# Optimization experiments

Hardware: AMD Instinct MI355X
Metric: run time of the kernel (lower is better)

## Reference

```python
import jax, jax.numpy as jnp
import numpy as np

B, N, H, D, L = 4, 1024, 8, 256, 4
SVD, NSP = 16, 512
DK = D // H
EPS = 1e-6


def setup_inputs() -> dict:
    key = jax.random.key(0)
    ks = jax.random.split(key, 40)
    p = {}
    p["x"] = jax.random.normal(ks[0], (B, N, D), jnp.float32)
    p["in_degrees"] = jax.random.randint(ks[1], (N,), 0, N)
    p["out_degrees"] = jax.random.randint(ks[2], (N,), 0, N)
    p["spatial_pos"] = jax.random.randint(ks[3], (N, N), 0, NSP)
    p["svd_emb"] = jax.random.normal(ks[4], (N, 2 * SVD), jnp.float32)
    # embedding tables (padding_idx=0 -> zero row)
    p["in_deg_emb"] = (0.02 * jax.random.normal(ks[5], (N, D), jnp.float32)).at[0].set(0.0)
    p["out_deg_emb"] = (0.02 * jax.random.normal(ks[6], (N, D), jnp.float32)).at[0].set(0.0)
    p["spatial_emb"] = (0.02 * jax.random.normal(ks[7], (NSP, H), jnp.float32)).at[0].set(0.0)
    # SVD linear (stored [in, out]; y = x @ W + b)
    p["W_svd"] = 0.02 * jax.random.normal(ks[8], (2 * SVD, D), jnp.float32)
    p["b_svd"] = jnp.zeros((D,), jnp.float32)
    # per-layer stacked transformer params
    names = ["Wq", "Wk", "Wv", "Wa", "W1", "W2"]
    for i, nm in enumerate(names):
        p[nm] = 0.05 * jax.random.normal(ks[9 + i], (L, D, D), jnp.float32)
    for nm in ["bq", "bk", "bv", "ba", "b1", "b2", "ln1_b", "ln2_b"]:
        p[nm] = jnp.zeros((L, D), jnp.float32)
    p["ln1_g"] = jnp.ones((L, D), jnp.float32)
    p["ln2_g"] = jnp.ones((L, D), jnp.float32)
    return p


def _ln(x, g, b):
    mu = jnp.mean(x, axis=-1, keepdims=True)
    var = jnp.mean(jnp.square(x - mu), axis=-1, keepdims=True)
    return (x - mu) * jax.lax.rsqrt(var + EPS) * g + b


def _forward(x, svd_emb, W_svd, b_svd, in_deg_emb, out_deg_emb, spatial_emb,
             Wq, bq, Wk, bk, Wv, bv, Wa, ba, ln1_g, ln1_b,
             W1, b1, W2, b2, ln2_g, ln2_b,
             in_degrees, out_degrees, spatial_pos):
    # node-level: degree embeddings ([N,D] broadcasts over batch)
    x = x + in_deg_emb[in_degrees] + out_deg_emb[out_degrees]
    # node-level: SVD embedding (deterministic sign = +1 -> concat(u, -v))
    pos = jnp.concatenate([svd_emb[:, :SVD], -svd_emb[:, SVD:]], axis=-1)
    x = x + pos @ W_svd + b_svd
    # attention-level spatial bias: [N,N,H] -> [H,N,N], broadcast over batch
    attn_bias = jnp.transpose(spatial_emb[spatial_pos], (2, 0, 1))
    scale = 1.0 / jnp.sqrt(jnp.asarray(DK, x.dtype))

    def body(h, params):
        wq, bq_, wk, bk_, wv, bv_, wa, ba_, g1, b1_, w1, bb1, w2, bb2, g2, b2_ = params
        q = (h @ wq + bq_).reshape(B, N, H, DK)
        k = (h @ wk + bk_).reshape(B, N, H, DK)
        v = (h @ wv + bv_).reshape(B, N, H, DK)
        # scores [B,H,N,N] + spatial bias [H,N,N]
        scores = jnp.einsum('bqhd,bkhd->bhqk', q, k) * scale + attn_bias
        attn = jax.nn.softmax(scores, axis=-1)
        o = jnp.einsum('bhqk,bkhd->bqhd', attn, v).reshape(B, N, D)
        h = _ln(h + o @ wa + ba_, g1, b1_)
        f = jnp.maximum(h @ w1 + bb1, 0.0) @ w2 + bb2
        h = _ln(h + f, g2, b2_)
        return h, None

    x, _ = jax.lax.scan(body, x, (Wq, bq, Wk, bk, Wv, bv, Wa, ba, ln1_g, ln1_b,
                                  W1, b1, W2, b2, ln2_g, ln2_b))
    return x


def reference(x, svd_emb, W_svd, b_svd, in_deg_emb, out_deg_emb, spatial_emb,
              Wq, bq, Wk, bk, Wv, bv, Wa, ba, ln1_g, ln1_b,
              W1, b1, W2, b2, ln2_g, ln2_b,
              in_degrees, out_degrees, spatial_pos):
    return _forward(x, svd_emb, W_svd, b_svd, in_deg_emb, out_deg_emb, spatial_emb,
                    Wq, bq, Wk, bk, Wv, bv, Wa, ba, ln1_g, ln1_b,
                    W1, b1, W2, b2, ln2_g, ln2_b,
                    in_degrees, out_degrees, spatial_pos)
```

## Files before the change

kernel.cpp:

```cpp
#include <hip/hip_runtime.h>
#include <hip/hip_bf16.h>
#include <math.h>

#define NN 1024
#define BB 4
#define HH 8
#define DD 256
#define LL 4
#define DKK 32
#define MM 4096
#define EPSF 1e-6f
#define LOG2EF 1.4426950408889634f
#define SCLOG2E 0.2550348625f

typedef __attribute__((ext_vector_type(8))) short short8;
typedef __attribute__((ext_vector_type(4))) float f32x4;
typedef unsigned int u32;

__device__ __forceinline__ unsigned short f2bf(float f) {
    __hip_bfloat16 h = __float2bfloat16(f);
    return *(unsigned short*)&h;
}
__device__ __forceinline__ float bf2f(unsigned short u) {
    unsigned v = ((unsigned)u) << 16;
    return __builtin_bit_cast(float, v);
}

__global__ __launch_bounds__(256) void init_kernel(
    const float* __restrict__ x, const int* __restrict__ deg_in,
    const int* __restrict__ deg_out, const float* __restrict__ svd,
    const float* __restrict__ in_emb, const float* __restrict__ out_emb,
    const float* __restrict__ Wsvd, const float* __restrict__ bsvd,
    const float* __restrict__ Wq, const float* __restrict__ Wk,
    const float* __restrict__ Wv, const float* __restrict__ Wa,
    const float* __restrict__ W1, const float* __restrict__ W2,
    const int* __restrict__ sp, const float* __restrict__ spemb,
    float* __restrict__ h, short* __restrict__ hb,
    short* __restrict__ Wt, short* __restrict__ bsw)
{
    int blk = blockIdx.x;
    int tid = threadIdx.x;
    {
        int n = blk & (NN - 1);
        int di = deg_in[n], dou = deg_out[n];
        float acc = x[(size_t)blk * DD + tid] + in_emb[(size_t)di * DD + tid]
                  + out_emb[(size_t)dou * DD + tid] + bsvd[tid];
        const float* sv = &svd[n * 32];
#pragma unroll
        for (int j = 0; j < 32; ++j) {
            float v = sv[j];
            v = (j < 16) ? v : -v;
            acc += v * Wsvd[j * DD + tid];
        }
        h[(size_t)blk * DD + tid] = acc;
        hb[(size_t)blk * DD + tid] = (short)f2bf(acc);
    }
    if (blk < 384) {
        __shared__ float t[64][65];
        int z = blk >> 4, tile = blk & 15;
        int name = z >> 2;
        const float* srcs[6] = {Wq, Wk, Wv, Wa, W1, W2};
        const float* W = srcs[name] + (size_t)(z & 3) * DD * DD;
        short* dst = Wt + (size_t)z * DD * DD;
        int r0 = (tile >> 2) * 64, c0 = (tile & 3) * 64;
#pragma unroll
        for (int i = 0; i < 16; ++i) {
            int idx = i * 256 + tid;
            int r = idx >> 6, cc = idx & 63;
            t[r][cc] = W[(size_t)(r0 + r) * DD + c0 + cc];
        }
        __syncthreads();
#pragma unroll
        for (int i = 0; i < 16; ++i) {
            int idx = i * 256 + tid;
            int n = idx >> 6, kk = idx & 63;
            dst[(size_t)(c0 + n) * DD + r0 + kk] = (short)f2bf(t[kk][n]);
        }
    } else if (blk < 1408) {
        int bb = blk - 384;
        int part = bb & 3;
        int tt = (bb >> 2) * 256 + tid;
        int ln = tt & 63, kt = (tt >> 6) & 15, q16 = tt >> 10;
        int qd = ln >> 4, cc = ln & 15;
        int row = q16 * 16 + cc;
        unsigned buf[8][2];
#pragma unroll
        for (int r = 0; r < 4; ++r) {
            int colj = kt * 64 + part * 16 + qd * 4 + r;
            int pp = sp[row * NN + colj];
            float4 e0 = *(const float4*)&spemb[pp * 8];
            float4 e1 = *(const float4*)&spemb[pp * 8 + 4];
            float ev[8] = {e0.x, e0.y, e0.z, e0.w, e1.x, e1.y, e1.z, e1.w};
#pragma unroll
            for (int hh = 0; hh < 8; ++hh) {
                unsigned short u = f2bf(ev[hh] * LOG2EF);
                if (r & 1) buf[hh][r >> 1] |= ((unsigned)u) << 16;
                else       buf[hh][r >> 1] = u;
            }
        }
#pragma unroll
        for (int hh = 0; hh < 8; ++hh) {
            uint2* dst = (uint2*)&bsw[(((size_t)hh * 64 + q16) * 16 + kt) * 1024
                                      + (size_t)ln * 16 + part * 4];
            *dst = make_uint2(buf[hh][0], buf[hh][1]);
        }
    }
}

__global__ __launch_bounds__(256) void gemm_qkv_kernel(
    const short* __restrict__ A,
    const short* __restrict__ Wtq, const short* __restrict__ Wtk,
    const short* __restrict__ Wtv,
    const float* __restrict__ bq, const float* __restrict__ bk,
    const float* __restrict__ bv,
    short* __restrict__ qo, short* __restrict__ ko, short* __restrict__ vo)
{
    int z = blockIdx.z;
    const short* Wt = (z == 0) ? Wtq : (z == 1) ? Wtk : Wtv;
    const float* bs = (z == 0) ? bq : (z == 1) ? bk : bv;
    int tid = threadIdx.x, wave = tid >> 6, lane = tid & 63;
    int quad = lane >> 4, c = lane & 15;
    int m0 = blockIdx.x * 16;
    int n0 = blockIdx.y * 64 + wave * 16;
    f32x4 acc = {0.f, 0.f, 0.f, 0.f};
    const short* Ap = &A[(size_t)(m0 + c) * DD];
#pragma unroll
    for (int ks = 0; ks < 8; ++ks) {
        short8 af = *(const short8*)&Ap[ks * 32 + quad * 8];
        short8 bf = *(const short8*)&Wt[(size_t)(n0 + c) * DD + ks * 32 + quad * 8];
        acc = __builtin_amdgcn_mfma_f32_16x16x32_bf16(af, bf, acc, 0, 0, 0);
    }
    int b = m0 >> 10;
    int tok0 = (m0 & (NN - 1)) + quad * 4;
    int col = n0 + c;
    int head = col >> 5, dk = col & 31;
    int bh = b * 8 + head;
    float bv2 = bs[col];
    if (z == 2) {
        ushort4 pk;
        pk.x = f2bf(acc[0] + bv2); pk.y = f2bf(acc[1] + bv2);
        pk.z = f2bf(acc[2] + bv2); pk.w = f2bf(acc[3] + bv2);
        *(ushort4*)&vo[((size_t)bh * DKK + dk) * NN + tok0] = pk;
    } else {
        short* out = (z == 0) ? qo : ko;
        float sc = (z == 0) ? SCLOG2E : 1.0f;
#pragma unroll
        for (int r = 0; r < 4; ++r)
            out[((size_t)bh * NN + tok0 + r) * DKK + dk] =
                (short)f2bf((acc[r] + bv2) * sc);
    }
}

__global__ __launch_bounds__(256) void attn_kernel(
    const short* __restrict__ q, const short* __restrict__ k,
    const short* __restrict__ vt, const short* __restrict__ bsw,
    short* __restrict__ obuf)
{
    int blk = blockIdx.x;
    int head = blk & 7;
    int b = (blk >> 3) & 3;
    int qg = blk >> 5;
    int tid = threadIdx.x, wave = tid >> 6, lane = tid & 63;
    int quad = lane >> 4, c = lane & 15;
    int bh = b * 8 + head;
    int qt = qg * 4 + wave;
    int q0 = qt * 16;
    int m0 = b * NN + q0;

    __shared__ short Ks[2][64][32];
    __shared__ short Vs[2][32][64];
    __shared__ short P[4][16][72];
    const f32x4 zero = {0.f, 0.f, 0.f, 0.f};

    auto stage = [&](int t, int buf) {
        const short* ksrc = &k[((size_t)bh * NN + t * 64 + wave * 16 + (lane >> 2)) * DKK
                               + (lane & 3) * 8];
        __builtin_amdgcn_global_load_lds(
            (const __attribute__((address_space(1))) u32*)ksrc,
            (__attribute__((address_space(3))) u32*)&Ks[buf][wave * 16][0], 16, 0, 0);
        const short* vsrc = &vt[((size_t)bh * DKK + wave * 8 + (lane >> 3)) * NN
                                + t * 64 + (lane & 7) * 8];
        __builtin_amdgcn_global_load_lds(
            (const __attribute__((address_space(1))) u32*)vsrc,
            (__attribute__((address_space(3))) u32*)&Vs[buf][wave * 8][0], 16, 0, 0);
    };

    stage(0, 0);

    short8 qf = *(const short8*)&q[((size_t)bh * NN + q0 + c) * DKK + quad * 8];
    const short* bbase = &bsw[(((size_t)head * 64 + qt) * 16) * 1024 + (size_t)lane * 16];
    short8 bc0 = *(const short8*)bbase;
    short8 bc1 = *(const short8*)(bbase + 8);

    f32x4 Oa0 = zero, Oa1 = zero;
    float lsum = 0.f;

    __syncthreads();

    for (int kti = 0; kti < 16; ++kti) {
        int cur = kti & 1;
        if (kti < 15) stage(kti + 1, cur ^ 1);
        short8 kf[4];
#pragma unroll
        for (int f = 0; f < 4; ++f)
            kf[f] = *(const short8*)&Ks[cur][f * 16 + c][quad * 8];
        short8 vf0[2], vf1[2];
#pragma unroll
        for (int kc = 0; kc < 2; ++kc) {
            vf0[kc] = *(const short8*)&Vs[cur][c][kc * 32 + quad * 8];
            vf1[kc] = *(const short8*)&Vs[cur][16 + c][kc * 32 + quad * 8];
        }
        f32x4 s[4];
#pragma unroll
        for (int f = 0; f < 4; ++f)
            s[f] = __builtin_amdgcn_mfma_f32_16x16x32_bf16(kf[f], qf, zero, 0, 0, 0);
        short8 bn0 = bc0, bn1 = bc1;
        if (kti < 15) {
            const short* bp = bbase + (size_t)(kti + 1) * 1024;
            bn0 = *(const short8*)bp;
            bn1 = *(const short8*)(bp + 8);
        }
#pragma unroll
        for (int f = 0; f < 4; ++f) {
            ushort4 pk;
#pragma unroll
            for (int r = 0; r < 4; ++r) {
                int jj = f * 4 + r;
                unsigned short uu = (unsigned short)((jj < 8) ? bc0[jj] : bc1[jj - 8]);
                float p = __builtin_amdgcn_exp2f(s[f][r] + bf2f(uu));
                lsum += p;
                unsigned short pb = f2bf(p);
                if (r == 0) pk.x = pb; else if (r == 1) pk.y = pb;
                else if (r == 2) pk.z = pb; else pk.w = pb;
            }
            *(ushort4*)&P[wave][c][f * 16 + quad * 4] = pk;
        }
        bc0 = bn0; bc1 = bn1;
#pragma unroll
        for (int kc = 0; kc < 2; ++kc) {
            short8 pf = *(const short8*)&P[wave][c][kc * 32 + quad * 8];
            Oa0 = __builtin_amdgcn_mfma_f32_16x16x32_bf16(pf, vf0[kc], Oa0, 0, 0, 0);
            Oa1 = __builtin_amdgcn_mfma_f32_16x16x32_bf16(pf, vf1[kc], Oa1, 0, 0, 0);
        }
        __syncthreads();
    }
    lsum += __shfl_xor(lsum, 16);
    lsum += __shfl_xor(lsum, 32);
#pragma unroll
    for (int r = 0; r < 4; ++r) {
        int rr = quad * 4 + r;
        float invl = 1.0f / __shfl(lsum, rr);
        obuf[(size_t)(m0 + rr) * DD + head * 32 + c]      = (short)f2bf(Oa0[r] * invl);
        obuf[(size_t)(m0 + rr) * DD + head * 32 + 16 + c] = (short)f2bf(Oa1[r] * invl);
    }
}

template <int QKV>
__global__ __launch_bounds__(512) void post_kernel(
    const short* __restrict__ obuf,
    const short* __restrict__ Wta, const short* __restrict__ Wt1,
    const short* __restrict__ Wt2,
    const float* __restrict__ ba, const float* __restrict__ b1,
    const float* __restrict__ b2,
    const float* __restrict__ g1, const float* __restrict__ lb1,
    const float* __restrict__ g2, const float* __restrict__ lb2,
    float* __restrict__ h,
    const short* __restrict__ Wtqn, const short* __restrict__ Wtkn,
    const short* __restrict__ Wtvn,
    const float* __restrict__ bqn, const float* __restrict__ bkn,
    const float* __restrict__ bvn,
    short* __restrict__ qo, short* __restrict__ ko, short* __restrict__ vo)
{
    int tid = threadIdx.x, wave = tid >> 6, lane = tid & 63;
    int quad = lane >> 4, c = lane & 15;
    int m0 = blockIdx.x * 16;
    int b = m0 >> 10;
    int q0 = m0 & (NN - 1);
    int nb = wave * 32;

    __shared__ short t_in[16][264];
    __shared__ short t1s[16][264];
    __shared__ float shs[8][16][2];
    const f32x4 zero = {0.f, 0.f, 0.f, 0.f};

    {
        int row = tid >> 5, cg = tid & 31;
        *(short8*)&t_in[row][cg * 8] = *(const short8*)&obuf[(size_t)(m0 + row) * DD + cg * 8];
    }
    __syncthreads();

    f32x4 acc[2] = {zero, zero};
#pragma unroll
    for (int ks = 0; ks < 8; ++ks) {
        short8 af = *(const short8*)&t_in[c][ks * 32 + quad * 8];
#pragma unroll
        for (int f = 0; f < 2; ++f) {
            short8 bf = *(const short8*)&Wta[(size_t)(nb + f * 16 + c) * DD + ks * 32 + quad * 8];
            acc[f] = __builtin_amdgcn_mfma_f32_16x16x32_bf16(af, bf, acc[f], 0, 0, 0);
        }
    }
    float val[2][4];
    float ps[4] = {0.f,0.f,0.f,0.f}, ps2[4] = {0.f,0.f,0.f,0.f};
#pragma unroll
    for (int f = 0; f < 2; ++f) {
        int col = nb + f * 16 + c;
        float bv = ba[col];
#pragma unroll
        for (int r = 0; r < 4; ++r) {
            float v = h[(size_t)(m0 + quad * 4 + r) * DD + col] + acc[f][r] + bv;
            val[f][r] = v;
            ps[r] += v;
            ps2[r] += v * v;
        }
    }
#pragma unroll
    for (int r = 0; r < 4; ++r)
#pragma unroll
        for (int off = 1; off < 16; off <<= 1) {
            ps[r]  += __shfl_xor(ps[r], off);
            ps2[r] += __shfl_xor(ps2[r], off);
        }
    if (c == 0)
#pragma unroll
        for (int r = 0; r < 4; ++r) {
            shs[wave][quad * 4 + r][0] = ps[r];
            shs[wave][quad * 4 + r][1] = ps2[r];
        }
    __syncthreads();
    float res[2][4];
#pragma unroll
    for (int r = 0; r < 4; ++r) {
        int rr = quad * 4 + r;
        float ts = 0.f, t2 = 0.f;
#pragma unroll
        for (int w = 0; w < 8; ++w) { ts += shs[w][rr][0]; t2 += shs[w][rr][1]; }
        float mu = ts * (1.0f / DD);
        float rv = rsqrtf(t2 * (1.0f / DD) - mu * mu + EPSF);
#pragma unroll
        for (int f = 0; f < 2; ++f) {
            int col = nb + f * 16 + c;
            float nv = (val[f][r] - mu) * rv * g1[col] + lb1[col];
            res[f][r] = nv;
            t_in[rr][col] = (short)f2bf(nv);
        }
    }
    __syncthreads();
#pragma unroll
    for (int f = 0; f < 2; ++f) {
        int n0 = nb + f * 16;
        f32x4 a1 = zero;
#pragma unroll
        for (int ks = 0; ks < 8; ++ks) {
            short8 af = *(const short8*)&t_in[c][ks * 32 + quad * 8];
            short8 bf = *(const short8*)&Wt1[(size_t)(n0 + c) * DD + ks * 32 + quad * 8];
            a1 = __builtin_amdgcn_mfma_f32_16x16x32_bf16(af, bf, a1, 0, 0, 0);
        }
        float bv = b1[n0 + c];
#pragma unroll
        for (int r = 0; r < 4; ++r)
            t1s[quad * 4 + r][n0 + c] = (short)f2bf(fmaxf(a1[r] + bv, 0.f));
    }
    __syncthreads();
    f32x4 acc2[2] = {zero, zero};
#pragma unroll
    for (int ks = 0; ks < 8; ++ks) {
        short8 af = *(const short8*)&t1s[c][ks * 32 + quad * 8];
#pragma unroll
        for (int f = 0; f < 2; ++f) {
            short8 bf = *(const short8*)&Wt2[(size_t)(nb + f * 16 + c) * DD + ks * 32 + quad * 8];
            acc2[f] = __builtin_amdgcn_mfma_f32_16x16x32_bf16(af, bf, acc2[f], 0, 0, 0);
        }
    }
    float ps_2[4] = {0.f,0.f,0.f,0.f}, ps2_2[4] = {0.f,0.f,0.f,0.f};
#pragma unroll
    for (int f = 0; f < 2; ++f) {
        int col = nb + f * 16 + c;
        float bv = b2[col];
#pragma unroll
        for (int r = 0; r < 4; ++r) {
            float v = res[f][r] + acc2[f][r] + bv;
            val[f][r] = v;
            ps_2[r] += v;
            ps2_2[r] += v * v;
        }
    }
#pragma unroll
    for (int r = 0; r < 4; ++r)
#pragma unroll
        for (int off = 1; off < 16; off <<= 1) {
            ps_2[r]  += __shfl_xor(ps_2[r], off);
            ps2_2[r] += __shfl_xor(ps2_2[r], off);
        }
    __syncthreads();
    if (c == 0)
#pragma unroll
        for (int r = 0; r < 4; ++r) {
            shs[wave][quad * 4 + r][0] = ps_2[r];
            shs[wave][quad * 4 + r][1] = ps2_2[r];
        }
    __syncthreads();
#pragma unroll
    for (int r = 0; r < 4; ++r) {
        int rr = quad * 4 + r;
        float ts = 0.f, t2 = 0.f;
#pragma unroll
        for (int w = 0; w < 8; ++w) { ts += shs[w][rr][0]; t2 += shs[w][rr][1]; }
        float mu = ts * (1.0f / DD);
        float rv = rsqrtf(t2 * (1.0f / DD) - mu * mu + EPSF);
#pragma unroll
        for (int f = 0; f < 2; ++f) {
            int col = nb + f * 16 + c;
            float nv = (val[f][r] - mu) * rv * g2[col] + lb2[col];
            h[(size_t)(m0 + rr) * DD + col] = nv;
            t_in[rr][col] = (short)f2bf(nv);
        }
    }
    if (QKV == 0) return;
    __syncthreads();
    {
        int tok0 = q0 + quad * 4;
        const short* Wz[3] = {Wtqn, Wtkn, Wtvn};
        const float* bz[3] = {bqn, bkn, bvn};
#pragma unroll
        for (int z = 0; z < 3; ++z) {
#pragma unroll
            for (int f = 0; f < 2; ++f) {
                int n0 = nb + f * 16;
                f32x4 aq = zero;
#pragma unroll
                for (int ks = 0; ks < 8; ++ks) {
                    short8 af = *(const short8*)&t_in[c][ks * 32 + quad * 8];
                    short8 bf = *(const short8*)&Wz[z][(size_t)(n0 + c) * DD + ks * 32 + quad * 8];
                    aq = __builtin_amdgcn_mfma_f32_16x16x32_bf16(af, bf, aq, 0, 0, 0);
                }
                int col = n0 + c;
                int hd = col >> 5, dk = col & 31;
                int bh2 = b * 8 + hd;
                float bv2 = bz[z][col];
                if (z == 2) {
                    ushort4 pk;
                    pk.x = f2bf(aq[0] + bv2); pk.y = f2bf(aq[1] + bv2);
                    pk.z = f2bf(aq[2] + bv2); pk.w = f2bf(aq[3] + bv2);
                    *(ushort4*)&vo[((size_t)bh2 * DKK + dk) * NN + tok0] = pk;
                } else {
                    short* out = (z == 0) ? qo : ko;
                    float sc = (z == 0) ? SCLOG2E : 1.0f;
#pragma unroll
                    for (int r = 0; r < 4; ++r)
                        out[((size_t)bh2 * NN + tok0 + r) * DKK + dk] =
                            (short)f2bf((aq[r] + bv2) * sc);
                }
            }
        }
    }
}

extern "C" void kernel_launch(void* const* d_in, const int* in_sizes, int n_in,
                              void* d_out, int out_size, void* d_ws, size_t ws_size,
                              hipStream_t stream)
{
    const float* x       = (const float*)d_in[0];
    const int*   deg_in  = (const int*)d_in[1];
    const int*   deg_out = (const int*)d_in[2];
    const int*   sp      = (const int*)d_in[3];
    const float* svd     = (const float*)d_in[4];
    const float* in_emb  = (const float*)d_in[5];
    const float* out_emb = (const float*)d_in[6];
    const float* spemb   = (const float*)d_in[7];
    const float* Wsvd    = (const float*)d_in[8];
    const float* bsvd    = (const float*)d_in[9];
    const float* Wq = (const float*)d_in[10];
    const float* Wk = (const float*)d_in[11];
    const float* Wv = (const float*)d_in[12];
    const float* Wa = (const float*)d_in[13];
    const float* W1 = (const float*)d_in[14];
    const float* W2 = (const float*)d_in[15];
    const float* bq = (const float*)d_in[16];
    const float* bk = (const float*)d_in[17];
    const float* bv = (const float*)d_in[18];
    const float* ba = (const float*)d_in[19];
    const float* b1 = (const float*)d_in[20];
    const float* b2 = (const float*)d_in[21];
    const float* ln1b = (const float*)d_in[22];
    const float* ln2b = (const float*)d_in[23];
    const float* ln1g = (const float*)d_in[24];
    const float* ln2g = (const float*)d_in[25];

    float* h = (float*)d_out;
    char*  ws = (char*)d_ws;
    short* bias = (short*)ws;
    short* qb   = (short*)(ws + ((size_t)16 << 20));
    short* kb   = (short*)(ws + ((size_t)18 << 20));
    short* vtb  = (short*)(ws + ((size_t)20 << 20));
    short* obuf = (short*)(ws + ((size_t)22 << 20));
    short* hb   = (short*)(ws + ((size_t)26 << 20));
    short* Wt   = (short*)(ws + ((size_t)28 << 20));

    init_kernel<<<MM, 256, 0, stream>>>(x, deg_in, deg_out, svd, in_emb,
        out_emb, Wsvd, bsvd, Wq, Wk, Wv, Wa, W1, W2, sp, spemb, h, hb, Wt, bias);

    const size_t WSZ = (size_t)DD * DD;
    gemm_qkv_kernel<<<dim3(MM / 16, 4, 3), 256, 0, stream>>>(
        hb, Wt + 0 * WSZ, Wt + 4 * WSZ, Wt + 8 * WSZ, bq, bk, bv, qb, kb, vtb);

    for (int l = 0; l < LL; ++l) {
        const size_t bo = (size_t)l * DD;
        const short* Wta = Wt + (3 * 4 + l) * WSZ;
        const short* Wt1 = Wt + (4 * 4 + l) * WSZ;
        const short* Wt2 = Wt + (5 * 4 + l) * WSZ;

        attn_kernel<<<512, 256, 0, stream>>>(qb, kb, vtb, bias, obuf);

        if (l < LL - 1) {
            const size_t bo_n = (size_t)(l + 1) * DD;
            post_kernel<1><<<MM / 16, 512, 0, stream>>>(
                obuf, Wta, Wt1, Wt2,
                ba + bo, b1 + bo, b2 + bo,
                ln1g + bo, ln1b + bo, ln2g + bo, ln2b + bo, h,
                Wt + (0 * 4 + l + 1) * WSZ, Wt + (1 * 4 + l + 1) * WSZ,
                Wt + (2 * 4 + l + 1) * WSZ,
                bq + bo_n, bk + bo_n, bv + bo_n, qb, kb, vtb);
        } else {
            post_kernel<0><<<MM / 16, 512, 0, stream>>>(
                obuf, Wta, Wt1, Wt2,
                ba + bo, b1 + bo, b2 + bo,
                ln1g + bo, ln1b + bo, ln2g + bo, ln2b + bo, h,
                nullptr, nullptr, nullptr, nullptr, nullptr, nullptr,
                nullptr, nullptr, nullptr);
        }
    }
}
```

Measured before the change: 324.7 us.

## Split QKV projection out of post kernel and halve attention block size

The fused QKV projection is removed from the post-attention kernel. The post kernel now writes a bf16 copy of h, and the existing gemm_qkv_kernel then computes Q/K/V for the next layer with its own wider grid. The attention kernel drops from 4 to 2 waves per block and launches 1024 blocks, so each wave stages two K/V segments. The aim is more parallelism and less serialized per-block work, at the cost of an extra launch and a round trip of h through global memory per layer, plus less K/V reuse per block.

Result: slower. 371.9 us (+14.5%).

```diff
diff --git a/kernel.cpp b/kernel.cpp
--- a/kernel.cpp
+++ b/kernel.cpp
@@ -151,7 +151,7 @@
     }
 }
 
-__global__ __launch_bounds__(256) void attn_kernel(
+__global__ __launch_bounds__(128) void attn_kernel(
     const short* __restrict__ q, const short* __restrict__ k,
     const short* __restrict__ vt, const short* __restrict__ bsw,
     short* __restrict__ obuf)
@@ -163,26 +163,30 @@
     int tid = threadIdx.x, wave = tid >> 6, lane = tid & 63;
     int quad = lane >> 4, c = lane & 15;
     int bh = b * 8 + head;
-    int qt = qg * 4 + wave;
+    int qt = qg * 2 + wave;
     int q0 = qt * 16;
     int m0 = b * NN + q0;
 
     __shared__ short Ks[2][64][32];
     __shared__ short Vs[2][32][64];
-    __shared__ short P[4][16][72];
+    __shared__ short P[2][16][72];
     const f32x4 zero = {0.f, 0.f, 0.f, 0.f};
 
     auto stage = [&](int t, int buf) {
-        const short* ksrc = &k[((size_t)bh * NN + t * 64 + wave * 16 + (lane >> 2)) * DKK
-                               + (lane & 3) * 8];
-        __builtin_amdgcn_global_load_lds(
-            (const __attribute__((address_space(1))) u32*)ksrc,
-            (__attribute__((address_space(3))) u32*)&Ks[buf][wave * 16][0], 16, 0, 0);
-        const short* vsrc = &vt[((size_t)bh * DKK + wave * 8 + (lane >> 3)) * NN
-                                + t * 64 + (lane & 7) * 8];
-        __builtin_amdgcn_global_load_lds(
-            (const __attribute__((address_space(1))) u32*)vsrc,
-            (__attribute__((address_space(3))) u32*)&Vs[buf][wave * 8][0], 16, 0, 0);
+#pragma unroll
+        for (int j = 0; j < 2; ++j) {
+            int seg = wave * 2 + j;
+            const short* ksrc = &k[((size_t)bh * NN + t * 64 + seg * 16 + (lane >> 2)) * DKK
+                                   + (lane & 3) * 8];
+            __builtin_amdgcn_global_load_lds(
+                (const __attribute__((address_space(1))) u32*)ksrc,
+                (__attribute__((address_space(3))) u32*)&Ks[buf][seg * 16][0], 16, 0, 0);
+            const short* vsrc = &vt[((size_t)bh * DKK + seg * 8 + (lane >> 3)) * NN
+                                    + t * 64 + (lane & 7) * 8];
+            __builtin_amdgcn_global_load_lds(
+                (const __attribute__((address_space(1))) u32*)vsrc,
+                (__attribute__((address_space(3))) u32*)&Vs[buf][seg * 8][0], 16, 0, 0);
+        }
     };
 
     stage(0, 0);
@@ -255,7 +259,6 @@
     }
 }
 
-template <int QKV>
 __global__ __launch_bounds__(512) void post_kernel(
     const short* __restrict__ obuf,
     const short* __restrict__ Wta, const short* __restrict__ Wt1,
@@ -264,18 +267,11 @@
     const float* __restrict__ b2,
     const float* __restrict__ g1, const float* __restrict__ lb1,
     const float* __restrict__ g2, const float* __restrict__ lb2,
-    float* __restrict__ h,
-    const short* __restrict__ Wtqn, const short* __restrict__ Wtkn,
-    const short* __restrict__ Wtvn,
-    const float* __restrict__ bqn, const float* __restrict__ bkn,
-    const float* __restrict__ bvn,
-    short* __restrict__ qo, short* __restrict__ ko, short* __restrict__ vo)
+    float* __restrict__ h, short* __restrict__ hb)
 {
     int tid = threadIdx.x, wave = tid >> 6, lane = tid & 63;
     int quad = lane >> 4, c = lane & 15;
     int m0 = blockIdx.x * 16;
-    int b = m0 >> 10;
-    int q0 = m0 & (NN - 1);
     int nb = wave * 32;
 
     __shared__ short t_in[16][264];
@@ -412,45 +408,7 @@
             int col = nb + f * 16 + c;
             float nv = (val[f][r] - mu) * rv * g2[col] + lb2[col];
             h[(size_t)(m0 + rr) * DD + col] = nv;
-            t_in[rr][col] = (short)f2bf(nv);
-        }
-    }
-    if (QKV == 0) return;
-    __syncthreads();
-    {
-        int tok0 = q0 + quad * 4;
-        const short* Wz[3] = {Wtqn, Wtkn, Wtvn};
-        const float* bz[3] = {bqn, bkn, bvn};
-#pragma unroll
-        for (int z = 0; z < 3; ++z) {
-#pragma unroll
-            for (int f = 0; f < 2; ++f) {
-                int n0 = nb + f * 16;
-                f32x4 aq = zero;
-#pragma unroll
-                for (int ks = 0; ks < 8; ++ks) {
-                    short8 af = *(const short8*)&t_in[c][ks * 32 + quad * 8];
-                    short8 bf = *(const short8*)&Wz[z][(size_t)(n0 + c) * DD + ks * 32 + quad * 8];
-                    aq = __builtin_amdgcn_mfma_f32_16x16x32_bf16(af, bf, aq, 0, 0, 0);
-                }
-                int col = n0 + c;
-                int hd = col >> 5, dk = col & 31;
-                int bh2 = b * 8 + hd;
-                float bv2 = bz[z][col];
-                if (z == 2) {
-                    ushort4 pk;
-                    pk.x = f2bf(aq[0] + bv2); pk.y = f2bf(aq[1] + bv2);
-                    pk.z = f2bf(aq[2] + bv2); pk.w = f2bf(aq[3] + bv2);
-                    *(ushort4*)&vo[((size_t)bh2 * DKK + dk) * NN + tok0] = pk;
-                } else {
-                    short* out = (z == 0) ? qo : ko;
-                    float sc = (z == 0) ? SCLOG2E : 1.0f;
-#pragma unroll
-                    for (int r = 0; r < 4; ++r)
-                        out[((size_t)bh2 * NN + tok0 + r) * DKK + dk] =
-                            (short)f2bf((aq[r] + bv2) * sc);
-                }
-            }
+            hb[(size_t)(m0 + rr) * DD + col] = (short)f2bf(nv);
         }
     }
 }
@@ -509,24 +467,19 @@
         const short* Wt1 = Wt + (4 * 4 + l) * WSZ;
         const short* Wt2 = Wt + (5 * 4 + l) * WSZ;
 
-        attn_kernel<<<512, 256, 0, stream>>>(qb, kb, vtb, bias, obuf);
+        attn_kernel<<<1024, 128, 0, stream>>>(qb, kb, vtb, bias, obuf);
+
+        post_kernel<<<MM / 16, 512, 0, stream>>>(
+            obuf, Wta, Wt1, Wt2,
+            ba + bo, b1 + bo, b2 + bo,
+            ln1g + bo, ln1b + bo, ln2g + bo, ln2b + bo, h, hb);
 
         if (l < LL - 1) {
             const size_t bo_n = (size_t)(l + 1) * DD;
-            post_kernel<1><<<MM / 16, 512, 0, stream>>>(
-                obuf, Wta, Wt1, Wt2,
-                ba + bo, b1 + bo, b2 + bo,
-                ln1g + bo, ln1b + bo, ln2g + bo, ln2b + bo, h,
-                Wt + (0 * 4 + l + 1) * WSZ, Wt + (1 * 4 + l + 1) * WSZ,
+            gemm_qkv_kernel<<<dim3(MM / 16, 4, 3), 256, 0, stream>>>(
+                hb, Wt + (0 * 4 + l + 1) * WSZ, Wt + (1 * 4 + l + 1) * WSZ,
                 Wt + (2 * 4 + l + 1) * WSZ,
                 bq + bo_n, bk + bo_n, bv + bo_n, qb, kb, vtb);
-        } else {
-            post_kernel<0><<<MM / 16, 512, 0, stream>>>(
-                obuf, Wta, Wt1, Wt2,
-                ba + bo, b1 + bo, b2 + bo,
-                ln1g + bo, ln1b + bo, ln2g + bo, ln2b + bo, h,
-                nullptr, nullptr, nullptr, nullptr, nullptr, nullptr,
-                nullptr, nullptr, nullptr);
-        }
-    }
-}
+        }
+    }
+}
```
